# Performance work log

Hardware: AMD Instinct MI355X
Metric: run time of the kernel (lower is better)

The kernel has to match this reference:

```python
import jax, jax.numpy as jnp
import numpy as np

N_NODES = 100000
N_EDGES = 800000
N_REL = 16
D = 64
EPS = 1e-12
NEG_SLOPE = 0.01  # nn.LeakyReLU default


def _l2norm(x):
    # matches torch F.normalize(p=2, dim=-1)
    n = jnp.sqrt(jnp.sum(x * x, axis=-1, keepdims=True))
    return x / jnp.maximum(n, EPS)


def setup_inputs() -> dict:
    key = jax.random.key(0)
    ks = jax.random.split(key, 12)
    inp = {
        "src": jax.random.randint(ks[0], (N_EDGES,), 0, N_NODES, dtype=jnp.int32),
        "dst": jax.random.randint(ks[1], (N_EDGES,), 0, N_NODES, dtype=jnp.int32),
        "etype": jax.random.randint(ks[2], (N_EDGES,), 0, N_REL, dtype=jnp.int32),
        "ent_embed": jax.random.normal(ks[3], (N_NODES, D), jnp.float32) * 0.1,
        "ent_transfer": jax.random.normal(ks[4], (N_NODES, D), jnp.float32) * 0.1,
        "rel_embed": jax.random.normal(ks[5], (N_REL, D), jnp.float32) * 0.1,
        "rel_transfer": jax.random.normal(ks[6], (N_REL, D), jnp.float32) * 0.1,
        "W1_0": jax.random.normal(ks[7], (64, 32), jnp.float32) * (1.0 / np.sqrt(64)),
        "b1_0": jnp.zeros((32,), jnp.float32),
        "W2_0": jax.random.normal(ks[8], (64, 32), jnp.float32) * (1.0 / np.sqrt(64)),
        "b2_0": jnp.zeros((32,), jnp.float32),
        "W1_1": jax.random.normal(ks[9], (32, 16), jnp.float32) * (1.0 / np.sqrt(32)),
        "b1_1": jnp.zeros((16,), jnp.float32),
        "W2_1": jax.random.normal(ks[10], (32, 16), jnp.float32) * (1.0 / np.sqrt(32)),
        "b2_1": jnp.zeros((16,), jnp.float32),
    }
    return inp


def _compute_att(src, dst, etype, ent_embed, ent_transfer, rel_embed, rel_transfer):
    # per-edge gathers: h = dst node, t = src node (KGAT att_score convention)
    h_e = ent_embed[dst]          # [E, D]
    t_e = ent_embed[src]          # [E, D]
    h_p = ent_transfer[dst]
    t_p = ent_transfer[src]
    r_p = rel_transfer[etype]     # [E, D]
    r_e = rel_embed[etype]        # [E, D]
    # TransD projection + L2 normalize
    Mrt = _l2norm(t_e + jnp.sum(t_e * t_p, -1, keepdims=True) * r_p)
    Mrh = _l2norm(h_e + jnp.sum(h_e * h_p, -1, keepdims=True) * r_p)
    att = jnp.sum(Mrt * jnp.tanh(Mrh + r_e), axis=-1)  # [E]
    # edge softmax grouped by destination node
    m = jax.ops.segment_max(att, dst, num_segments=N_NODES)
    m = jnp.where(jnp.isfinite(m), m, 0.0)
    ex = jnp.exp(att - m[dst])
    s = jax.ops.segment_sum(ex, dst, num_segments=N_NODES)
    return ex / jnp.maximum(s[dst], EPS)  # [E]


def _bi_layer(node, N_h, W1, b1, W2, b2):
    out1 = jax.nn.leaky_relu((node + N_h) @ W1 + b1, NEG_SLOPE)
    out2 = jax.nn.leaky_relu((node * N_h) @ W2 + b2, NEG_SLOPE)
    return out1 + out2


def reference(src, dst, etype, ent_embed, ent_transfer, rel_embed, rel_transfer,
              W1_0, b1_0, W2_0, b2_0, W1_1, b1_1, W2_1, b2_1):
    att = _compute_att(src, dst, etype, ent_embed, ent_transfer, rel_embed, rel_transfer)
    node = ent_embed
    all_embed = [node]
    for (W1, b1, W2, b2) in [(W1_0, b1_0, W2_0, b2_0), (W1_1, b1_1, W2_1, b2_1)]:
        # u_mul_e + sum: N_h[v] = sum_{e: dst(e)=v} att_e * node[src(e)]
        msg = att[:, None] * node[src]                      # [E, d]
        N_h = jax.ops.segment_sum(msg, dst, num_segments=N_NODES)
        node = _bi_layer(node, N_h, W1, b1, W2, b2)         # dropout p=0 (eval)
        all_embed.append(_l2norm(node))
    return jnp.concatenate(all_embed, axis=1)  # [N, 64+32+16]
```

## Files before the change

### kernel.cpp

```cpp
#include <hip/hip_runtime.h>
#include <math.h>

#define EPSF 1e-12f
#define LOG2E 1.44269504f

template <int CTRL>
__device__ __forceinline__ float dppadd(float x) {
    union { float f; int i; } u, r;
    u.f = x;
    r.i = __builtin_amdgcn_update_dpp(0, u.i, CTRL, 0xF, 0xF, false);
    return x + r.f;
}
__device__ __forceinline__ float red16(float v) {
    v = dppadd<0xB1>(v); v = dppadd<0x4E>(v);
    v = dppadd<0x141>(v); v = dppadd<0x140>(v);
    return v;
}
__device__ __forceinline__ float red8(float v) {
    v = dppadd<0xB1>(v); v = dppadd<0x4E>(v); v = dppadd<0x141>(v);
    return v;
}
__device__ __forceinline__ float xor8add(float v) {
    return dppadd<0x128>(v);
}

__device__ __forceinline__ float fast_tanh(float x) {
    float E = __builtin_amdgcn_exp2f(x * (2.0f * LOG2E));
    return 1.0f - 2.0f * __builtin_amdgcn_rcpf(E + 1.0f);
}

__device__ __forceinline__ float inv_norm(float x) {
    return __builtin_amdgcn_rsqf(fmaxf(x, 1e-24f));
}

__device__ __forceinline__ float leaky(float x) {
    return x > 0.0f ? x : 0.01f * x;
}

__global__ __launch_bounds__(256) void prep(
    const float* __restrict__ ent, const float* __restrict__ entT,
    float2* __restrict__ dn, const int* __restrict__ dst,
    int* __restrict__ deg, int N16, int E,
    const float* __restrict__ relT, float* __restrict__ hrp,
    float* __restrict__ rp2,
    const float* __restrict__ W10, const float* __restrict__ W20,
    const float* __restrict__ W11, const float* __restrict__ W21,
    float4* __restrict__ wt) {
    __shared__ float rTl[16][64];
    int t = threadIdx.x;
    {
        int r = t >> 4, c = (t & 15) * 4;
        *(float4*)&rTl[r][c] = *(const float4*)(relT + r * 64 + c);
    }
    __syncthreads();

    int gid = blockIdx.x * 256 + t;
    if (gid < N16) {
        int v = gid >> 4, lane = gid & 15;
        const float4 a = *(const float4*)(ent  + (size_t)v * 64 + lane * 4);
        const float4 b = *(const float4*)(entT + (size_t)v * 64 + lane * 4);
        float d  = red16(a.x*b.x + a.y*b.y + a.z*b.z + a.w*b.w);
        float n2 = red16(a.x*a.x + a.y*a.y + a.z*a.z + a.w*a.w);
        if (lane == 0) dn[v] = make_float2(d, n2);
        #pragma unroll
        for (int r = 0; r < 16; ++r) {
            const float4 w = *(const float4*)&rTl[r][lane * 4];
            float p = a.x*w.x + a.y*w.y + a.z*w.z + a.w*w.w;
            p = red16(p);
            if (lane == r) hrp[(size_t)v * 16 + r] = p;
        }
    } else if (gid < N16 + E) {
        int e = gid - N16;
        atomicAdd(&deg[dst[e]], 1);
    } else if (gid < N16 + E + 16) {
        int r = gid - N16 - E;
        const float4* w4 = (const float4*)(relT + r * 64);
        float acc = 0.0f;
        #pragma unroll
        for (int k = 0; k < 16; ++k) {
            float4 b = w4[k];
            acc += b.x*b.x + b.y*b.y + b.z*b.z + b.w*b.w;
        }
        rp2[r] = acc;
    } else {
        int w = gid - N16 - E - 16;
        if (w < 512) {
            int dd = w >> 5, j = w & 31, d4 = dd * 4;
            wt[w] = make_float4(W10[(d4+0)*32+j], W10[(d4+1)*32+j],
                                W10[(d4+2)*32+j], W10[(d4+3)*32+j]);
        } else if (w < 1024) {
            int u = w - 512, dd = u >> 5, j = u & 31, d4 = dd * 4;
            wt[w] = make_float4(W20[(d4+0)*32+j], W20[(d4+1)*32+j],
                                W20[(d4+2)*32+j], W20[(d4+3)*32+j]);
        } else if (w < 1152) {
            int u = w - 1024, dd = u >> 4, j = u & 15, d4 = dd * 4;
            wt[w] = make_float4(W11[(d4+0)*16+j], W11[(d4+1)*16+j],
                                W11[(d4+2)*16+j], W11[(d4+3)*16+j]);
        } else if (w < 1280) {
            int u = w - 1152, dd = u >> 4, j = u & 15, d4 = dd * 4;
            wt[w] = make_float4(W21[(d4+0)*16+j], W21[(d4+1)*16+j],
                                W21[(d4+2)*16+j], W21[(d4+3)*16+j]);
        }
    }
}


__global__ __launch_bounds__(256) void scan_reduce(
    const int* __restrict__ deg, int* __restrict__ part, int N) {
    __shared__ int sh[256];
    int t = threadIdx.x, i = blockIdx.x * 256 + t;
    sh[t] = (i < N) ? deg[i] : 0;
    __syncthreads();
    for (int off = 128; off > 0; off >>= 1) {
        if (t < off) sh[t] += sh[t + off];
        __syncthreads();
    }
    if (t == 0) part[blockIdx.x] = sh[0];
}

__global__ __launch_bounds__(1024) void scan_part(int* __restrict__ part, int nb) {
    __shared__ int sh[1024];
    int t = threadIdx.x;
    int x = (t < nb) ? part[t] : 0;
    sh[t] = x;
    __syncthreads();
    for (int off = 1; off < 1024; off <<= 1) {
        int y = (t >= off) ? sh[t - off] : 0;
        __syncthreads();
        sh[t] += y;
        __syncthreads();
    }
    if (t < nb) part[t] = sh[t] - x;
}

__global__ __launch_bounds__(256) void scan_write(
    int* __restrict__ rowptr, const int* __restrict__ part, int N) {
    __shared__ int sh[256];
    int t = threadIdx.x, i = blockIdx.x * 256 + t;
    int x = (i < N) ? rowptr[i] : 0;
    sh[t] = x;
    __syncthreads();
    for (int off = 1; off < 256; off <<= 1) {
        int y = (t >= off) ? sh[t - off] : 0;
        __syncthreads();
        sh[t] += y;
        __syncthreads();
    }
    if (i < N) rowptr[i] = part[blockIdx.x] + sh[t] - x;
}

__global__ __launch_bounds__(256) void scatter_edges(
    const int* __restrict__ src, const int* __restrict__ dst,
    const int* __restrict__ ety, const float2* __restrict__ dn,
    const float* __restrict__ hrp, const float* __restrict__ rp2,
    int* __restrict__ rowptr, int4* __restrict__ spk4, int E) {
    int e = blockIdx.x * 256 + threadIdx.x;
    if (e < E) {
        int sv = src[e], dv = dst[e], rv = ety[e];
        float2 dns = dn[sv], dnd = dn[dv];
        float hs = hrp[(size_t)sv * 16 + rv], hd = hrp[(size_t)dv * 16 + rv];
        float r2 = rp2[rv];
        float sdt = dns.x, dh = dnd.x;
        float sst = dns.y + 2.0f * sdt * hs + sdt * sdt * r2;
        float ssh = dnd.y + 2.0f * dh  * hd + dh  * dh  * r2;
        float it = inv_norm(sst);
        float ih = inv_norm(ssh);
        int slot = atomicAdd(&rowptr[dv], 1);
        spk4[slot] = make_int4(sv | (rv << 20), __float_as_int(sdt),
                               __float_as_int(it), __float_as_int(ih));
    }
}

__global__ __launch_bounds__(256) void fused_l0(
    const int* __restrict__ rowptr, const int4* __restrict__ spk4,
    const float* __restrict__ ent, const float2* __restrict__ dn,
    const float* __restrict__ relE, const float* __restrict__ relT,
    const float4* __restrict__ wt,
    const float* __restrict__ b1, const float* __restrict__ b2,
    float* __restrict__ exatt, float* __restrict__ sinv,
    float* __restrict__ node1raw, float* __restrict__ out, int N) {
    __shared__ float  al[8][64];
    __shared__ float  bl[8][64];
    __shared__ float  rT[16][64];
    __shared__ float  rE[16][64];
    __shared__ float4 WtA[512];
    __shared__ float4 WtB[512];
    int t = threadIdx.x;

    {
        int r = t >> 4, c = (t & 15) * 4;
        *(float4*)&rT[r][c] = *(const float4*)(relT + r * 64 + c);
        *(float4*)&rE[r][c] = *(const float4*)(relE + r * 64 + c);
        WtA[t]       = wt[t];
        WtA[t + 256] = wt[t + 256];
        WtB[t]       = wt[512 + t];
        WtB[t + 256] = wt[768 + t];
    }
    __syncthreads();

    int nv = t >> 5, half = (t >> 4) & 1, lane = t & 15;
    int v = blockIdx.x * 8 + nv;
    if (v >= N) return;

    int s = v ? rowptr[v - 1] : 0;
    int epos = rowptr[v];
    int deg = epos - s;
    int mid = s + ((deg + 1) >> 1);
    int hs   = half ? mid  : s;
    int hend = half ? epos : mid;

    const float4 he = *(const float4*)(ent + (size_t)v * 64 + lane * 4);
    float dh = dn[v].x;

    float4 macc = {0.f, 0.f, 0.f, 0.f};
    float sumex = 0.0f;

    for (int base = hs; base < hend; base += 16) {
        int rem = hend - base;
        int cnt = rem < 16 ? rem : 16;
        int4 ms = spk4[base + (lane < rem ? lane : rem - 1)];
        float myex = 0.0f;

        int e1i = cnt > 1 ? 1 : 0;
        int   pk0 = __shfl(ms.x, 0, 16);
        int   pk1 = __shfl(ms.x, e1i, 16);
        float sd0 = __int_as_float(__shfl(ms.y, 0, 16));
        float sd1 = __int_as_float(__shfl(ms.y, e1i, 16));
        float it0 = __int_as_float(__shfl(ms.z, 0, 16));
        float it1 = __int_as_float(__shfl(ms.z, e1i, 16));
        float ih0 = __int_as_float(__shfl(ms.w, 0, 16));
        float ih1 = __int_as_float(__shfl(ms.w, e1i, 16));
        float4 te0 = *(const float4*)(ent + (size_t)(pk0 & 0xFFFFF) * 64 + lane * 4);
        float4 te1 = *(const float4*)(ent + (size_t)(pk1 & 0xFFFFF) * 64 + lane * 4);

        for (int k = 0; k < cnt; k += 2) {
            float4 ta = te0, tb = te1;
            float  sa = sd0, sb = sd1;
            float ita = it0, itb = it1, iha = ih0, ihb = ih1;
            int rva = (pk0 >> 20) & 15;
            int rvb = (pk1 >> 20) & 15;
            bool hasb = (k + 1) < cnt;

            if (k + 2 < cnt) {
                int i2 = k + 2, i3 = (k + 3 < cnt) ? (k + 3) : (k + 2);
                pk0 = __shfl(ms.x, i2, 16);
                pk1 = __shfl(ms.x, i3, 16);
                sd0 = __int_as_float(__shfl(ms.y, i2, 16));
                sd1 = __int_as_float(__shfl(ms.y, i3, 16));
                it0 = __int_as_float(__shfl(ms.z, i2, 16));
                it1 = __int_as_float(__shfl(ms.z, i3, 16));
                ih0 = __int_as_float(__shfl(ms.w, i2, 16));
                ih1 = __int_as_float(__shfl(ms.w, i3, 16));
                te0 = *(const float4*)(ent + (size_t)(pk0 & 0xFFFFF) * 64 + lane * 4);
                te1 = *(const float4*)(ent + (size_t)(pk1 & 0xFFFFF) * 64 + lane * 4);
            }

            const float4 rpa = *(const float4*)&rT[rva][lane * 4];
            const float4 rea = *(const float4*)&rE[rva][lane * 4];
            const float4 rpb = *(const float4*)&rT[rvb][lane * 4];
            const float4 reb = *(const float4*)&rE[rvb][lane * 4];

            float4 mta, mha, mtb, mhb;
            mta.x = ta.x + sa * rpa.x; mta.y = ta.y + sa * rpa.y;
            mta.z = ta.z + sa * rpa.z; mta.w = ta.w + sa * rpa.w;
            mha.x = he.x + dh * rpa.x; mha.y = he.y + dh * rpa.y;
            mha.z = he.z + dh * rpa.z; mha.w = he.w + dh * rpa.w;
            mtb.x = tb.x + sb * rpb.x; mtb.y = tb.y + sb * rpb.y;
            mtb.z = tb.z + sb * rpb.z; mtb.w = tb.w + sb * rpb.w;
            mhb.x = he.x + dh * rpb.x; mhb.y = he.y + dh * rpb.y;
            mhb.z = he.z + dh * rpb.z; mhb.w = he.w + dh * rpb.w;

            float txa = fast_tanh(mha.x * iha + rea.x);
            float tya = fast_tanh(mha.y * iha + rea.y);
            float tza = fast_tanh(mha.z * iha + rea.z);
            float twa = fast_tanh(mha.w * iha + rea.w);
            float txb = fast_tanh(mhb.x * ihb + reb.x);
            float tyb = fast_tanh(mhb.y * ihb + reb.y);
            float tzb = fast_tanh(mhb.z * ihb + reb.z);
            float twb = fast_tanh(mhb.w * ihb + reb.w);

            float atta = ita * red16(mta.x*txa + mta.y*tya + mta.z*tza + mta.w*twa);
            float attb = itb * red16(mtb.x*txb + mtb.y*tyb + mtb.z*tzb + mtb.w*twb);

            float exa  = __builtin_amdgcn_exp2f(atta * LOG2E);
            float exbR = __builtin_amdgcn_exp2f(attb * LOG2E);
            float exb  = hasb ? exbR : 0.0f;

            myex = (lane == k) ? exa : myex;
            myex = (lane == k + 1) ? exbR : myex;

            sumex += exa + exb;
            macc.x += exa * ta.x + exb * tb.x;
            macc.y += exa * ta.y + exb * tb.y;
            macc.z += exa * ta.z + exb * tb.z;
            macc.w += exa * ta.w + exb * tb.w;
        }
        if (lane < cnt) exatt[base + lane] = myex;
    }

    sumex  += __shfl_xor(sumex,  16, 32);
    macc.x += __shfl_xor(macc.x, 16, 32);
    macc.y += __shfl_xor(macc.y, 16, 32);
    macc.z += __shfl_xor(macc.z, 16, 32);
    macc.w += __shfl_xor(macc.w, 16, 32);

    float inv = 1.0f / fmaxf(sumex, EPSF);
    if ((t & 31) == 0) sinv[v] = inv;
    macc.x *= inv; macc.y *= inv; macc.z *= inv; macc.w *= inv;

    if (!half) {
        *(float4*)(out + (size_t)v * 112 + lane * 4) = he;
        float4 av, bv;
        av.x = he.x + macc.x; av.y = he.y + macc.y;
        av.z = he.z + macc.z; av.w = he.w + macc.w;
        bv.x = he.x * macc.x; bv.y = he.y * macc.y;
        bv.z = he.z * macc.z; bv.w = he.w * macc.w;
        *(float4*)&al[nv][lane * 4] = av;
        *(float4*)&bl[nv][lane * 4] = bv;
    }

    int j = t & 31;
    float acc1 = b1[j], acc2 = b2[j];
    #pragma unroll
    for (int dd = 0; dd < 16; ++dd) {
        float4 a4 = *(const float4*)&al[nv][dd * 4];
        float4 b4 = *(const float4*)&bl[nv][dd * 4];
        float4 wa = WtA[dd * 32 + j];
        float4 wb = WtB[dd * 32 + j];
        acc1 += a4.x*wa.x + a4.y*wa.y + a4.z*wa.z + a4.w*wa.w;
        acc2 += b4.x*wb.x + b4.y*wb.y + b4.z*wb.z + b4.w*wb.w;
    }
    node1raw[(size_t)v * 32 + j] = leaky(acc1) + leaky(acc2);
}

__global__ __launch_bounds__(256) void fused_l1(
    const int* __restrict__ rowptr, const int4* __restrict__ spk4,
    const float* __restrict__ exatt, const float* __restrict__ sinv,
    const float* __restrict__ node1raw, const float4* __restrict__ wt,
    const float* __restrict__ b1, const float* __restrict__ b2,
    float* __restrict__ out, int N) {
    __shared__ float  A[16][32];
    __shared__ float  B[16][32];
    __shared__ float4 WtC[128];
    __shared__ float4 WtD[128];
    int t = threadIdx.x;

    {
        if (t < 128) WtC[t] = wt[1024 + t];
        else WtD[t - 128] = wt[1024 + t];
    }
    __syncthreads();

    int nv = t >> 4, half = (t >> 3) & 1, lane = t & 7;
    int v = blockIdx.x * 16 + nv;
    if (v >= N) return;

    int s = v ? rowptr[v - 1] : 0;
    int epos = rowptr[v];
    int deg = epos - s;
    int mid = s + ((deg + 1) >> 1);
    int hs   = half ? mid  : s;
    int hend = half ? epos : mid;

    float4 n = *(const float4*)(node1raw + (size_t)v * 32 + lane * 4);
    float4 acc = {0.f, 0.f, 0.f, 0.f};

    for (int base = hs; base < hend; base += 8) {
        int rem = hend - base;
        int cnt = rem < 8 ? rem : 8;
        int idx = base + (lane < rem ? lane : rem - 1);
        int   mypk = spk4[idx].x;
        float myex = exatt[idx];

        int pk0 = __shfl(mypk, 0, 8);
        int pk1 = __shfl(mypk, cnt > 1 ? 1 : 0, 8);
        float4 x0 = *(const float4*)(node1raw + (size_t)(pk0 & 0xFFFFF) * 32 + lane * 4);
        float4 x1 = *(const float4*)(node1raw + (size_t)(pk1 & 0xFFFFF) * 32 + lane * 4);

        for (int k = 0; k < cnt; k += 2) {
            float4 xa = x0, xb = x1;
            float aa = __shfl(myex, k, 8);
            float ab = __shfl(myex, (k + 1 < cnt) ? (k + 1) : k, 8);
            if (!((k + 1) < cnt)) ab = 0.0f;

            if (k + 2 < cnt) {
                pk0 = __shfl(mypk, k + 2, 8);
                pk1 = __shfl(mypk, (k + 3 < cnt) ? (k + 3) : (k + 2), 8);
                x0 = *(const float4*)(node1raw + (size_t)(pk0 & 0xFFFFF) * 32 + lane * 4);
                x1 = *(const float4*)(node1raw + (size_t)(pk1 & 0xFFFFF) * 32 + lane * 4);
            }
            acc.x += aa * xa.x + ab * xb.x;
            acc.y += aa * xa.y + ab * xb.y;
            acc.z += aa * xa.z + ab * xb.z;
            acc.w += aa * xa.w + ab * xb.w;
        }
    }
    acc.x = xor8add(acc.x);
    acc.y = xor8add(acc.y);
    acc.z = xor8add(acc.z);
    acc.w = xor8add(acc.w);

    float inv = sinv[v];
    acc.x *= inv; acc.y *= inv; acc.z *= inv; acc.w *= inv;

    float ss = red8(n.x*n.x + n.y*n.y + n.z*n.z + n.w*n.w);
    float inv1 = inv_norm(ss);

    if (!half) {
        float4 nn = {n.x*inv1, n.y*inv1, n.z*inv1, n.w*inv1};
        *(float4*)(out + (size_t)v * 112 + 64 + lane * 4) = nn;
        float4 av = {n.x + acc.x, n.y + acc.y, n.z + acc.z, n.w + acc.w};
        float4 bv = {n.x * acc.x, n.y * acc.y, n.z * acc.z, n.w * acc.w};
        *(float4*)&A[nv][lane * 4] = av;
        *(float4*)&B[nv][lane * 4] = bv;
    }

    int j = t & 15;
    float a1 = b1[j], a2 = b2[j];
    #pragma unroll
    for (int dd = 0; dd < 8; ++dd) {
        float4 a4 = *(const float4*)&A[nv][dd * 4];
        float4 b4 = *(const float4*)&B[nv][dd * 4];
        float4 wc = WtC[dd * 16 + j];
        float4 wd = WtD[dd * 16 + j];
        a1 += a4.x*wc.x + a4.y*wc.y + a4.z*wc.z + a4.w*wc.w;
        a2 += b4.x*wd.x + b4.y*wd.y + b4.z*wd.z + b4.w*wd.w;
    }
    float tot = leaky(a1) + leaky(a2);
    float s2 = red16(tot * tot);
    float inv2 = inv_norm(s2);
    out[(size_t)v * 112 + 96 + j] = tot * inv2;
}

extern "C" void kernel_launch(void* const* d_in, const int* in_sizes, int n_in,
                              void* d_out, int out_size, void* d_ws, size_t ws_size,
                              hipStream_t stream) {
    const int*   src  = (const int*)d_in[0];
    const int*   dst  = (const int*)d_in[1];
    const int*   ety  = (const int*)d_in[2];
    const float* ent  = (const float*)d_in[3];
    const float* entT = (const float*)d_in[4];
    const float* relE = (const float*)d_in[5];
    const float* relT = (const float*)d_in[6];
    const float* W1_0 = (const float*)d_in[7];
    const float* b1_0 = (const float*)d_in[8];
    const float* W2_0 = (const float*)d_in[9];
    const float* b2_0 = (const float*)d_in[10];
    const float* W1_1 = (const float*)d_in[11];
    const float* b1_1 = (const float*)d_in[12];
    const float* W2_1 = (const float*)d_in[13];
    const float* b2_1 = (const float*)d_in[14];
    float* out = (float*)d_out;

    const int E = in_sizes[0];
    const int N = in_sizes[3] / 64;
    const int nb = (N + 255) / 256;

    auto al256 = [](size_t x) { return (x + 255) & ~(size_t)255; };
    char* ws = (char*)d_ws;
    size_t offExatt = 0;
    size_t offDn    = al256(offExatt + (size_t)E * 4);
    size_t offS     = al256(offDn + (size_t)N * 8);
    size_t offRow   = al256(offS + (size_t)N * 4);
    size_t offSpk   = al256(offRow + (size_t)N * 4);
    size_t offHrp   = al256(offSpk + (size_t)E * 16);
    size_t offRp2   = al256(offHrp + (size_t)N * 16 * 4);
    size_t offPart  = al256(offRp2 + 16 * 4);
    size_t offN1    = al256(offPart + (size_t)nb * 4);
    size_t offWt    = al256(offN1 + (size_t)N * 32 * 4);
    float*  exatt    = (float*)(ws + offExatt);
    float2* dn       = (float2*)(ws + offDn);
    float*  sinv     = (float*)(ws + offS);
    int*    rowptr   = (int*)(ws + offRow);
    int4*   spk4     = (int4*)(ws + offSpk);
    float*  hrp      = (float*)(ws + offHrp);
    float*  rp2      = (float*)(ws + offRp2);
    int*    part     = (int*)(ws + offPart);
    float*  node1raw = (float*)(ws + offN1);
    float4* wt       = (float4*)(ws + offWt);

    hipMemsetAsync(rowptr, 0, (size_t)N * 4, stream);
    int N16 = N * 16;
    int prepWork = N16 + E + 16 + 1280;
    prep<<<(prepWork + 255) / 256, 256, 0, stream>>>(
        ent, entT, dn, dst, rowptr, N16, E, relT, hrp, rp2,
        W1_0, W2_0, W1_1, W2_1, wt);
    scan_reduce<<<nb, 256, 0, stream>>>(rowptr, part, N);
    scan_part<<<1, 1024, 0, stream>>>(part, nb);
    scan_write<<<nb, 256, 0, stream>>>(rowptr, part, N);
    int blkE = (E + 255) / 256;
    scatter_edges<<<blkE, 256, 0, stream>>>(src, dst, ety, dn, hrp, rp2,
                                            rowptr, spk4, E);

    fused_l0<<<(N + 7) / 8, 256, 0, stream>>>(
        rowptr, spk4, ent, dn, relE, relT,
        wt, b1_0, b2_0, exatt, sinv, node1raw, out, N);

    fused_l1<<<(N + 15) / 16, 256, 0, stream>>>(
        rowptr, spk4, exatt, sinv, node1raw, wt,
        b1_1, b2_1, out, N);
}
```

Before: 203.2 us.

## Replace cooperative edge-metadata load and shuffles with per-edge broadcast loads

Both fused kernels stop loading 16/8 edge records cooperatively and distributing them with lane shuffles. Each lane now loads the edge record (and, in layer 1, the attention value) directly from memory, with a two-edge prefetch. Layer 0 drops the LDS staging of the weight matrices, reads them from global/cache inside a partially unrolled loop, and has lane 0 write the exp scores per edge. This removes shuffle overhead and shared-memory footprint, but adds redundant uniform global loads, serialized dependent load chains, and many small scalar stores.

```diff
diff --git a/kernel.cpp b/kernel.cpp
--- a/kernel.cpp
+++ b/kernel.cpp
@@ -179,22 +179,16 @@
     const float* __restrict__ b1, const float* __restrict__ b2,
     float* __restrict__ exatt, float* __restrict__ sinv,
     float* __restrict__ node1raw, float* __restrict__ out, int N) {
-    __shared__ float  al[8][64];
-    __shared__ float  bl[8][64];
-    __shared__ float  rT[16][64];
-    __shared__ float  rE[16][64];
-    __shared__ float4 WtA[512];
-    __shared__ float4 WtB[512];
+    __shared__ float al[8][64];
+    __shared__ float bl[8][64];
+    __shared__ float rT[16][64];
+    __shared__ float rE[16][64];
     int t = threadIdx.x;
 
     {
         int r = t >> 4, c = (t & 15) * 4;
         *(float4*)&rT[r][c] = *(const float4*)(relT + r * 64 + c);
         *(float4*)&rE[r][c] = *(const float4*)(relE + r * 64 + c);
-        WtA[t]       = wt[t];
-        WtA[t + 256] = wt[t + 256];
-        WtB[t]       = wt[512 + t];
-        WtB[t + 256] = wt[768 + t];
     }
     __syncthreads();
 
@@ -215,45 +209,32 @@
     float4 macc = {0.f, 0.f, 0.f, 0.f};
     float sumex = 0.0f;
 
-    for (int base = hs; base < hend; base += 16) {
-        int rem = hend - base;
-        int cnt = rem < 16 ? rem : 16;
-        int4 ms = spk4[base + (lane < rem ? lane : rem - 1)];
-        float myex = 0.0f;
-
-        int e1i = cnt > 1 ? 1 : 0;
-        int   pk0 = __shfl(ms.x, 0, 16);
-        int   pk1 = __shfl(ms.x, e1i, 16);
-        float sd0 = __int_as_float(__shfl(ms.y, 0, 16));
-        float sd1 = __int_as_float(__shfl(ms.y, e1i, 16));
-        float it0 = __int_as_float(__shfl(ms.z, 0, 16));
-        float it1 = __int_as_float(__shfl(ms.z, e1i, 16));
-        float ih0 = __int_as_float(__shfl(ms.w, 0, 16));
-        float ih1 = __int_as_float(__shfl(ms.w, e1i, 16));
-        float4 te0 = *(const float4*)(ent + (size_t)(pk0 & 0xFFFFF) * 64 + lane * 4);
-        float4 te1 = *(const float4*)(ent + (size_t)(pk1 & 0xFFFFF) * 64 + lane * 4);
-
-        for (int k = 0; k < cnt; k += 2) {
-            float4 ta = te0, tb = te1;
-            float  sa = sd0, sb = sd1;
-            float ita = it0, itb = it1, iha = ih0, ihb = ih1;
-            int rva = (pk0 >> 20) & 15;
-            int rvb = (pk1 >> 20) & 15;
-            bool hasb = (k + 1) < cnt;
-
-            if (k + 2 < cnt) {
-                int i2 = k + 2, i3 = (k + 3 < cnt) ? (k + 3) : (k + 2);
-                pk0 = __shfl(ms.x, i2, 16);
-                pk1 = __shfl(ms.x, i3, 16);
-                sd0 = __int_as_float(__shfl(ms.y, i2, 16));
-                sd1 = __int_as_float(__shfl(ms.y, i3, 16));
-                it0 = __int_as_float(__shfl(ms.z, i2, 16));
-                it1 = __int_as_float(__shfl(ms.z, i3, 16));
-                ih0 = __int_as_float(__shfl(ms.w, i2, 16));
-                ih1 = __int_as_float(__shfl(ms.w, i3, 16));
-                te0 = *(const float4*)(ent + (size_t)(pk0 & 0xFFFFF) * 64 + lane * 4);
-                te1 = *(const float4*)(ent + (size_t)(pk1 & 0xFFFFF) * 64 + lane * 4);
+    if (hs < hend) {
+        int last = hend - 1;
+        int iB = (hs + 1 <= last) ? hs + 1 : last;
+        int4 pA = spk4[hs];
+        int4 pB = spk4[iB];
+        float4 teA = *(const float4*)(ent + (size_t)(pA.x & 0xFFFFF) * 64 + lane * 4);
+        float4 teB = *(const float4*)(ent + (size_t)(pB.x & 0xFFFFF) * 64 + lane * 4);
+
+        for (int k = hs; k < hend; k += 2) {
+            int4 cA = pA, cB = pB;
+            float4 ta = teA, tb = teB;
+            bool hasb = (k + 1) < hend;
+
+            if (k + 2 < hend) {
+                int j1 = (k + 3 <= last) ? k + 3 : last;
+                pA = spk4[k + 2];
+                pB = spk4[j1];
+                teA = *(const float4*)(ent + (size_t)(pA.x & 0xFFFFF) * 64 + lane * 4);
+                teB = *(const float4*)(ent + (size_t)(pB.x & 0xFFFFF) * 64 + lane * 4);
             }
+
+            float sa = __int_as_float(cA.y), sb = __int_as_float(cB.y);
+            float ita = __int_as_float(cA.z), itb = __int_as_float(cB.z);
+            float iha = __int_as_float(cA.w), ihb = __int_as_float(cB.w);
+            int rva = (cA.x >> 20) & 15;
+            int rvb = (cB.x >> 20) & 15;
 
             const float4 rpa = *(const float4*)&rT[rva][lane * 4];
             const float4 rea = *(const float4*)&rE[rva][lane * 4];
@@ -286,16 +267,16 @@
             float exbR = __builtin_amdgcn_exp2f(attb * LOG2E);
             float exb  = hasb ? exbR : 0.0f;
 
-            myex = (lane == k) ? exa : myex;
-            myex = (lane == k + 1) ? exbR : myex;
-
+            if (lane == 0) {
+                exatt[k] = exa;
+                if (hasb) exatt[k + 1] = exbR;
+            }
             sumex += exa + exb;
             macc.x += exa * ta.x + exb * tb.x;
             macc.y += exa * ta.y + exb * tb.y;
             macc.z += exa * ta.z + exb * tb.z;
             macc.w += exa * ta.w + exb * tb.w;
         }
-        if (lane < cnt) exatt[base + lane] = myex;
     }
 
     sumex  += __shfl_xor(sumex,  16, 32);
@@ -321,12 +302,12 @@
 
     int j = t & 31;
     float acc1 = b1[j], acc2 = b2[j];
-    #pragma unroll
+    #pragma unroll 4
     for (int dd = 0; dd < 16; ++dd) {
         float4 a4 = *(const float4*)&al[nv][dd * 4];
         float4 b4 = *(const float4*)&bl[nv][dd * 4];
-        float4 wa = WtA[dd * 32 + j];
-        float4 wb = WtB[dd * 32 + j];
+        float4 wa = wt[dd * 32 + j];
+        float4 wb = wt[512 + dd * 32 + j];
         acc1 += a4.x*wa.x + a4.y*wa.y + a4.z*wa.z + a4.w*wa.w;
         acc2 += b4.x*wb.x + b4.y*wb.y + b4.z*wb.z + b4.w*wb.w;
     }
@@ -365,29 +346,29 @@
     float4 n = *(const float4*)(node1raw + (size_t)v * 32 + lane * 4);
     float4 acc = {0.f, 0.f, 0.f, 0.f};
 
-    for (int base = hs; base < hend; base += 8) {
-        int rem = hend - base;
-        int cnt = rem < 8 ? rem : 8;
-        int idx = base + (lane < rem ? lane : rem - 1);
-        int   mypk = spk4[idx].x;
-        float myex = exatt[idx];
-
-        int pk0 = __shfl(mypk, 0, 8);
-        int pk1 = __shfl(mypk, cnt > 1 ? 1 : 0, 8);
-        float4 x0 = *(const float4*)(node1raw + (size_t)(pk0 & 0xFFFFF) * 32 + lane * 4);
-        float4 x1 = *(const float4*)(node1raw + (size_t)(pk1 & 0xFFFFF) * 32 + lane * 4);
-
-        for (int k = 0; k < cnt; k += 2) {
-            float4 xa = x0, xb = x1;
-            float aa = __shfl(myex, k, 8);
-            float ab = __shfl(myex, (k + 1 < cnt) ? (k + 1) : k, 8);
-            if (!((k + 1) < cnt)) ab = 0.0f;
-
-            if (k + 2 < cnt) {
-                pk0 = __shfl(mypk, k + 2, 8);
-                pk1 = __shfl(mypk, (k + 3 < cnt) ? (k + 3) : (k + 2), 8);
-                x0 = *(const float4*)(node1raw + (size_t)(pk0 & 0xFFFFF) * 32 + lane * 4);
-                x1 = *(const float4*)(node1raw + (size_t)(pk1 & 0xFFFFF) * 32 + lane * 4);
+    if (hs < hend) {
+        int last = hend - 1;
+        int iB = (hs + 1 <= last) ? hs + 1 : last;
+        int   pkA = spk4[hs].x;
+        int   pkB = spk4[iB].x;
+        float exA = exatt[hs];
+        float exB = exatt[iB];
+        float4 xA = *(const float4*)(node1raw + (size_t)(pkA & 0xFFFFF) * 32 + lane * 4);
+        float4 xB = *(const float4*)(node1raw + (size_t)(pkB & 0xFFFFF) * 32 + lane * 4);
+
+        for (int k = hs; k < hend; k += 2) {
+            float4 xa = xA, xb = xB;
+            float aa = exA;
+            float ab = ((k + 1) < hend) ? exB : 0.0f;
+
+            if (k + 2 < hend) {
+                int j1 = (k + 3 <= last) ? k + 3 : last;
+                pkA = spk4[k + 2].x;
+                pkB = spk4[j1].x;
+                exA = exatt[k + 2];
+                exB = exatt[j1];
+                xA = *(const float4*)(node1raw + (size_t)(pkA & 0xFFFFF) * 32 + lane * 4);
+                xB = *(const float4*)(node1raw + (size_t)(pkB & 0xFFFFF) * 32 + lane * 4);
             }
             acc.x += aa * xa.x + ab * xb.x;
             acc.y += aa * xa.y + ab * xb.y;
```

After: 218.1 us. +7.4%, slower.
